# Kernel optimization log

Hardware: AMD Instinct MI355X
Metric: run time of the kernel (lower is better)

Reference implementation:

```python
import jax, jax.numpy as jnp
import numpy as np

N_NODES = 50000
N_EDGES = 800000
D_IN = 128
D_HID = 128
D_OUT = 64


def sage_conv(x, edge_index, W_l, b_l, W_r):
    # PyG SAGEConv (mean aggr): out = lin_l(mean_{j in N(i)} x_j) + lin_r(x_i)
    src, dst = edge_index[0], edge_index[1]
    msgs = x[src]  # [E, d] gather of source-node features
    summed = jax.ops.segment_sum(msgs, dst, num_segments=x.shape[0])
    deg = jax.ops.segment_sum(jnp.ones((edge_index.shape[1],), x.dtype), dst,
                              num_segments=x.shape[0])
    agg = summed / jnp.maximum(deg, 1.0)[:, None]  # nodes w/o in-edges -> 0
    return agg @ W_l + b_l + x @ W_r


def setup_inputs() -> dict:
    key = jax.random.key(0)
    ks = jax.random.split(key, 12)
    x = jax.random.normal(ks[0], (N_NODES, D_IN), dtype=jnp.float32)
    edge_index = jax.random.randint(ks[1], (2, N_EDGES), 0, N_NODES, dtype=jnp.int32)

    def glorot(k, shape):
        fan_in, fan_out = shape
        lim = (6.0 / (fan_in + fan_out)) ** 0.5
        return jax.random.uniform(k, shape, jnp.float32, -lim, lim)

    dims = [(D_IN, D_HID), (D_HID, D_HID), (D_HID, D_OUT)]
    params = {}
    for i, (din, dout) in enumerate(dims):
        params[f"Wl{i}"] = glorot(ks[2 + 3 * i], (din, dout))
        params[f"bl{i}"] = jnp.zeros((dout,), jnp.float32)
        params[f"Wr{i}"] = glorot(ks[3 + 3 * i], (din, dout))
    return {"x": x, "edge_index": edge_index, **params}


def reference(x, edge_index, Wl0, bl0, Wr0, Wl1, bl1, Wr1, Wl2, bl2, Wr2):
    # eval mode: dropout is identity
    h = jax.nn.relu(sage_conv(x, edge_index, Wl0, bl0, Wr0))
    h = jax.nn.relu(sage_conv(h, edge_index, Wl1, bl1, Wr1))
    out = sage_conv(h, edge_index, Wl2, bl2, Wr2)
    return out
```

## Files before the change

kernel.cpp:

```cpp
#include <hip/hip_runtime.h>

#define NN 50000
#define NE 800000
#define DK 128
#define NN_PAD 50048

#define SW 7
#define SUBCAP 20
#define CAP2 64

#define NPB 128
#define NBKT 391
#define BKTCAP 4096

#define AGG_BLOCKS 1568

typedef __attribute__((ext_vector_type(8))) short bf16x8;
typedef __attribute__((ext_vector_type(4))) float f32x4;
typedef __attribute__((ext_vector_type(2))) int   i32x2;
typedef __attribute__((ext_vector_type(4))) int   i32x4;
typedef __attribute__((ext_vector_type(4))) unsigned u32x4;
typedef __attribute__((ext_vector_type(8))) unsigned short u16x8;

__device__ inline unsigned short f2bf(float f) {
    unsigned u = __builtin_bit_cast(unsigned, f);
    u = (u + 0x7FFFu + ((u >> 16) & 1u)) >> 16;
    return (unsigned short)u;
}
__device__ inline float bfhi2f(unsigned u) {
    return __builtin_bit_cast(float, u & 0xFFFF0000u);
}
__device__ inline float bflo2f(unsigned u) {
    return __builtin_bit_cast(float, u << 16);
}
__device__ inline int clampn(int v) {
    return v >= NN ? NN - 1 : v;
}
__device__ inline void acc16(float* acc, u32x4 v) {
    acc[0] += bflo2f(v.x); acc[1] += bfhi2f(v.x);
    acc[2] += bflo2f(v.y); acc[3] += bfhi2f(v.y);
    acc[4] += bflo2f(v.z); acc[5] += bfhi2f(v.z);
    acc[6] += bflo2f(v.w); acc[7] += bfhi2f(v.w);
}


__global__ __launch_bounds__(256) void zero_int(int* __restrict__ p, int n) {
    int i = blockIdx.x * 256 + threadIdx.x;
    if (i < n) p[i] = 0;
}

__global__ __launch_bounds__(256) void partition_edges(const int* __restrict__ src,
                                                       const int* __restrict__ dst,
                                                       int* __restrict__ gcount,
                                                       unsigned* __restrict__ bucketbuf) {
    __shared__ int hist[NBKT];
    __shared__ int cur[NBKT];
    __shared__ int base[NBKT];
    int tid = threadIdx.x;
    for (int i = tid; i < NBKT; i += 256) { hist[i] = 0; cur[i] = 0; }
    __syncthreads();

    unsigned rec[8];
    int bkt[8];
    int e0 = (blockIdx.x * 256 + tid) * 8;
    bool valid = e0 < NE;
    if (valid) {
        i32x4 sa = __builtin_nontemporal_load((const i32x4*)(src + e0));
        i32x4 sb = __builtin_nontemporal_load((const i32x4*)(src + e0 + 4));
        i32x4 da = __builtin_nontemporal_load((const i32x4*)(dst + e0));
        i32x4 db = __builtin_nontemporal_load((const i32x4*)(dst + e0 + 4));
        int ss[8] = {sa.x, sa.y, sa.z, sa.w, sb.x, sb.y, sb.z, sb.w};
        int dd[8] = {da.x, da.y, da.z, da.w, db.x, db.y, db.z, db.w};
        #pragma unroll
        for (int k = 0; k < 8; ++k) {
            bkt[k] = dd[k] >> 7;
            rec[k] = (unsigned)ss[k] | ((unsigned)(dd[k] & 127) << 16);
            atomicAdd(&hist[bkt[k]], 1);
        }
    }
    __syncthreads();
    for (int i = tid; i < NBKT; i += 256)
        base[i] = atomicAdd(&gcount[i], hist[i]);
    __syncthreads();
    if (valid) {
        #pragma unroll
        for (int k = 0; k < 8; ++k) {
            int pos = base[bkt[k]] + atomicAdd(&cur[bkt[k]], 1);
            if (pos < BKTCAP)
                bucketbuf[(size_t)bkt[k] * BKTCAP + pos] = rec[k];
        }
    }
}

__global__ __launch_bounds__(256) void build_lists(const int* __restrict__ gcount,
                                                   const unsigned* __restrict__ bucketbuf,
                                                   unsigned short* __restrict__ eidx2,
                                                   int* __restrict__ deg) {
    __shared__ unsigned short list[NPB * CAP2];
    __shared__ int cnt[NPB * 8];
    __shared__ int cur[NPB * 8];
    __shared__ int off_[NPB * 8];
    int b = blockIdx.x, tid = threadIdx.x;
    int n0 = b << 7;
    int cntE = gcount[b];
    if (cntE > BKTCAP) cntE = BKTCAP;

    for (int i = tid; i < NPB * 8; i += 256) { cnt[i] = 0; cur[i] = 0; }
    u32x4* l4 = (u32x4*)list;
    for (int i = tid; i < NPB * CAP2 / 8; i += 256)
        l4[i] = (u32x4){0u, 0u, 0u, 0u};
    __syncthreads();

    const unsigned* bb = bucketbuf + (size_t)b * BKTCAP;
    for (int i = tid; i < cntE; i += 256) {
        unsigned r = bb[i];
        int nl = r >> 16;
        int w  = (r & 0xFFFFu) >> 13;
        atomicAdd(&cnt[nl * 8 + w], 1);
    }
    __syncthreads();

    if (tid < NPB) {
        int run = 0, dt = 0;
        #pragma unroll
        for (int w = 0; w < SW; ++w) {
            int c = cnt[tid * 8 + w];
            dt += c;
            off_[tid * 8 + w] = run;
            run += (c < SUBCAP) ? c : SUBCAP;
        }
        if (n0 + tid < NN) deg[n0 + tid] = dt;
    }
    __syncthreads();

    for (int i = tid; i < cntE; i += 256) {
        unsigned r = bb[i];
        int s  = (int)(r & 0xFFFFu);
        int nl = r >> 16;
        int w  = s >> 13;
        int slot = atomicAdd(&cur[nl * 8 + w], 1);
        int pos  = off_[nl * 8 + w] + slot;
        if (slot < SUBCAP && pos < CAP2)
            list[nl * CAP2 + pos] = (unsigned short)s;
    }
    __syncthreads();

    int nvalid = NN - n0;
    if (nvalid > NPB) nvalid = NPB;
    u32x4* out4 = (u32x4*)(eidx2 + (size_t)n0 * CAP2);
    for (int i = tid; i < nvalid * (CAP2 / 8); i += 256)
        __builtin_nontemporal_store(l4[i], out4 + i);
}


__global__ __launch_bounds__(256) void convert_bf16(const float* __restrict__ x,
                                                    unsigned short* __restrict__ xb) {
    long long i = (long long)(blockIdx.x * 256 + threadIdx.x) * 8;
    if (i >= (long long)NN * DK) return;
    f32x4 a = __builtin_nontemporal_load((const f32x4*)(x + i));
    f32x4 b = __builtin_nontemporal_load((const f32x4*)(x + i + 4));
    union { unsigned short us[8]; u32x4 u4; } o;
    o.us[0] = f2bf(a.x); o.us[1] = f2bf(a.y); o.us[2] = f2bf(a.z); o.us[3] = f2bf(a.w);
    o.us[4] = f2bf(b.x); o.us[5] = f2bf(b.y); o.us[6] = f2bf(b.z); o.us[7] = f2bf(b.w);
    *(u32x4*)(xb + i) = o.u4;
}


__global__ __launch_bounds__(256) void pack_w(const float* __restrict__ Wl,
                                              const float* __restrict__ Wr,
                                              unsigned short* __restrict__ Wpack,
                                              int N) {
    int tid = blockIdx.x * 256 + threadIdx.x;
    if (tid >= N * 32) return;
    int l  = tid & 63;
    int ks = (tid >> 6) & 7;
    int nt = tid >> 9;
    int n  = nt * 16 + (l & 15);
    int kb = ks * 32 + (l >> 4) * 8;
    union { unsigned short us[8]; u32x4 u4; } o;
    #pragma unroll
    for (int j = 0; j < 8; ++j) {
        int k = kb + j;
        float w = (k < 128) ? Wl[k * N + n] : Wr[(k - 128) * N + n];
        o.us[j] = f2bf(w);
    }
    *(u32x4*)(Wpack + (size_t)tid * 8) = o.u4;
}

__global__ __launch_bounds__(256) void pack_w1(const float* __restrict__ W,
                                               unsigned short* __restrict__ Wpack) {
    int tid = blockIdx.x * 256 + threadIdx.x;
    if (tid >= 1024) return;
    int l  = tid & 63;
    int ks = (tid >> 6) & 3;
    int nt = tid >> 8;
    int n  = nt * 16 + (l & 15);
    int kb = ks * 32 + (l >> 4) * 8;
    union { unsigned short us[8]; u32x4 u4; } o;
    #pragma unroll
    for (int j = 0; j < 8; ++j) o.us[j] = f2bf(W[(kb + j) * 64 + n]);
    *(u32x4*)(Wpack + (size_t)tid * 8) = o.u4;
}

template <int S>
__global__ __launch_bounds__(256) void aggregate(const unsigned short* __restrict__ h,
                                                 const unsigned short* __restrict__ eidx2,
                                                 const int* __restrict__ deg,
                                                 unsigned short* __restrict__ agg) {
    constexpr int NPB_ = 256 / S;
    int g    = threadIdx.x / S;
    int lane = threadIdx.x % S;
    const u32x4* h4 = (const u32x4*)h;
    for (int base = 0; base < NN; base += AGG_BLOCKS * NPB_) {
        int node = base + blockIdx.x * NPB_ + g;
        if (node >= NN) continue;
        int d   = deg[node];
        int cap = (d < CAP2) ? d : CAP2;
        const unsigned short* el = eidx2 + (size_t)node * CAP2;
        float acc[8] = {0.f, 0.f, 0.f, 0.f, 0.f, 0.f, 0.f, 0.f};
        int j = 0;
        for (; j + 7 < cap; j += 8) {
            u16x8 i8 = *(const u16x8*)(el + j);
            u32x4 v[8];
            #pragma unroll
            for (int q = 0; q < 8; ++q)
                v[q] = h4[(size_t)clampn((int)i8[q]) * S + lane];
            #pragma unroll
            for (int q = 0; q < 8; ++q) acc16(acc, v[q]);
        }
        for (; j + 3 < cap; j += 4) {
            u32x4 v[4];
            #pragma unroll
            for (int q = 0; q < 4; ++q)
                v[q] = h4[(size_t)clampn((int)el[j + q]) * S + lane];
            #pragma unroll
            for (int q = 0; q < 4; ++q) acc16(acc, v[q]);
        }
        for (; j < cap; ++j)
            acc16(acc, h4[(size_t)clampn((int)el[j]) * S + lane]);
        float r = 1.0f / (float)(d > 0 ? d : 1);
        union { unsigned short us[8]; u32x4 u4; } o;
        #pragma unroll
        for (int k = 0; k < 8; ++k) o.us[k] = f2bf(acc[k] * r);
        __builtin_nontemporal_store(o.u4, (u32x4*)agg + (size_t)node * S + lane);
    }
}


template <int N, bool RELU, bool OUT_BF16>
__global__ __launch_bounds__(256) void gemm_mfma(const unsigned short* __restrict__ agg,
                                                 const unsigned short* __restrict__ h,
                                                 const unsigned short* __restrict__ Wpack,
                                                 const float* __restrict__ bias,
                                                 void* __restrict__ outp) {
    __shared__ unsigned short Wlds[N * 256];
    int tid = threadIdx.x;
    {
        const u32x4* wg = (const u32x4*)Wpack;
        u32x4* wl = (u32x4*)Wlds;
        #pragma unroll
        for (int i = tid; i < N * 32; i += 256) wl[i] = wg[i];
    }
    __syncthreads();

    int wave = tid >> 6, lane = tid & 63;
    int m = lane & 15, quad = lane >> 4;
    int row0 = blockIdx.x * 128 + wave * 16;

    const unsigned short* arow = agg + (size_t)(row0 + m) * 128 + quad * 8;
    const unsigned short* hrow = h   + (size_t)(row0 + m) * 128 + quad * 8;

    f32x4 acc0[N / 16] = {};
    f32x4 acc1[N / 16] = {};
    #pragma unroll
    for (int ks = 0; ks < 8; ++ks) {
        const unsigned short* s = (ks < 4) ? (arow + ks * 32) : (hrow + (ks - 4) * 32);
        bf16x8 a0 = *(const bf16x8*)s;
        bf16x8 a1 = *(const bf16x8*)(s + 64 * 128);
        #pragma unroll
        for (int nt = 0; nt < N / 16; ++nt) {
            bf16x8 b = *(const bf16x8*)&Wlds[((nt * 8 + ks) * 64 + lane) * 8];
            acc0[nt] = __builtin_amdgcn_mfma_f32_16x16x32_bf16(a0, b, acc0[nt], 0, 0, 0);
            acc1[nt] = __builtin_amdgcn_mfma_f32_16x16x32_bf16(a1, b, acc1[nt], 0, 0, 0);
        }
    }

    #pragma unroll
    for (int t = 0; t < 2; ++t) {
        #pragma unroll
        for (int nt = 0; nt < N / 16; ++nt) {
            int n = nt * 16 + m;
            float bv = bias[n];
            #pragma unroll
            for (int r = 0; r < 4; ++r) {
                int row = row0 + t * 64 + quad * 4 + r;
                if (row < NN) {
                    float v = (t == 0 ? acc0[nt][r] : acc1[nt][r]) + bv;
                    if (RELU) v = fmaxf(v, 0.f);
                    if (OUT_BF16)
                        ((unsigned short*)outp)[(size_t)row * N + n] = f2bf(v);
                    else
                        ((float*)outp)[(size_t)row * N + n] = v;
                }
            }
        }
    }
}

__global__ __launch_bounds__(256) void gemm_single(const unsigned short* __restrict__ h,
                                                   const unsigned short* __restrict__ Wpack,
                                                   unsigned short* __restrict__ P) {
    __shared__ unsigned short Wlds[64 * 128];
    int tid = threadIdx.x;
    {
        const u32x4* wg = (const u32x4*)Wpack;
        u32x4* wl = (u32x4*)Wlds;
        #pragma unroll
        for (int i = tid; i < 1024; i += 256) wl[i] = wg[i];
    }
    __syncthreads();

    int wave = tid >> 6, lane = tid & 63;
    int m = lane & 15, quad = lane >> 4;
    int row0 = blockIdx.x * 128 + wave * 16;

    const unsigned short* hrow = h + (size_t)(row0 + m) * 128 + quad * 8;

    f32x4 acc0[4] = {};
    f32x4 acc1[4] = {};
    #pragma unroll
    for (int ks = 0; ks < 4; ++ks) {
        bf16x8 a0 = *(const bf16x8*)(hrow + ks * 32);
        bf16x8 a1 = *(const bf16x8*)(hrow + ks * 32 + 64 * 128);
        #pragma unroll
        for (int nt = 0; nt < 4; ++nt) {
            bf16x8 b = *(const bf16x8*)&Wlds[((nt * 4 + ks) * 64 + lane) * 8];
            acc0[nt] = __builtin_amdgcn_mfma_f32_16x16x32_bf16(a0, b, acc0[nt], 0, 0, 0);
            acc1[nt] = __builtin_amdgcn_mfma_f32_16x16x32_bf16(a1, b, acc1[nt], 0, 0, 0);
        }
    }

    #pragma unroll
    for (int t = 0; t < 2; ++t) {
        #pragma unroll
        for (int nt = 0; nt < 4; ++nt) {
            int n = nt * 16 + m;
            #pragma unroll
            for (int r = 0; r < 4; ++r) {
                int row = row0 + t * 64 + quad * 4 + r;
                if (row < NN)
                    P[(size_t)row * 64 + n] = f2bf(t == 0 ? acc0[nt][r] : acc1[nt][r]);
            }
        }
    }
}

__global__ __launch_bounds__(256) void gemm_final(const unsigned short* __restrict__ h,
                                                  const unsigned short* __restrict__ Wpack,
                                                  const float* __restrict__ bias,
                                                  const unsigned short* __restrict__ aggP,
                                                  float* __restrict__ outp) {
    __shared__ unsigned short Wlds[64 * 128];
    int tid = threadIdx.x;
    {
        const u32x4* wg = (const u32x4*)Wpack;
        u32x4* wl = (u32x4*)Wlds;
        #pragma unroll
        for (int i = tid; i < 1024; i += 256) wl[i] = wg[i];
    }
    __syncthreads();

    int wave = tid >> 6, lane = tid & 63;
    int m = lane & 15, quad = lane >> 4;
    int row0 = blockIdx.x * 128 + wave * 16;

    const unsigned short* hrow = h + (size_t)(row0 + m) * 128 + quad * 8;

    f32x4 acc0[4] = {};
    f32x4 acc1[4] = {};
    #pragma unroll
    for (int ks = 0; ks < 4; ++ks) {
        bf16x8 a0 = *(const bf16x8*)(hrow + ks * 32);
        bf16x8 a1 = *(const bf16x8*)(hrow + ks * 32 + 64 * 128);
        #pragma unroll
        for (int nt = 0; nt < 4; ++nt) {
            bf16x8 b = *(const bf16x8*)&Wlds[((nt * 4 + ks) * 64 + lane) * 8];
            acc0[nt] = __builtin_amdgcn_mfma_f32_16x16x32_bf16(a0, b, acc0[nt], 0, 0, 0);
            acc1[nt] = __builtin_amdgcn_mfma_f32_16x16x32_bf16(a1, b, acc1[nt], 0, 0, 0);
        }
    }

    #pragma unroll
    for (int t = 0; t < 2; ++t) {
        #pragma unroll
        for (int nt = 0; nt < 4; ++nt) {
            int n = nt * 16 + m;
            float bv = bias[n];
            #pragma unroll
            for (int r = 0; r < 4; ++r) {
                int row = row0 + t * 64 + quad * 4 + r;
                if (row < NN) {
                    float av = bflo2f((unsigned)aggP[(size_t)row * 64 + n]);
                    outp[(size_t)row * 64 + n] =
                        (t == 0 ? acc0[nt][r] : acc1[nt][r]) + bv + av;
                }
            }
        }
    }
}


static inline size_t align256(size_t x) { return (x + 255) & ~(size_t)255; }

extern "C" void kernel_launch(void* const* d_in, const int* in_sizes, int n_in,
                              void* d_out, int out_size, void* d_ws, size_t ws_size,
                              hipStream_t stream) {
    const float* x    = (const float*)d_in[0];
    const int*   ei   = (const int*)d_in[1];
    const int*   esrc = ei;
    const int*   edst = ei + NE;
    const float* Wl0 = (const float*)d_in[2];
    const float* bl0 = (const float*)d_in[3];
    const float* Wr0 = (const float*)d_in[4];
    const float* Wl1 = (const float*)d_in[5];
    const float* bl1 = (const float*)d_in[6];
    const float* Wr1 = (const float*)d_in[7];
    const float* Wl2 = (const float*)d_in[8];
    const float* bl2 = (const float*)d_in[9];
    const float* Wr2 = (const float*)d_in[10];

    char* ws = (char*)d_ws;
    size_t off = 0;
    int* gcount = (int*)(ws + off);             off = align256(off + (size_t)NBKT * 4);
    unsigned* bucketbuf = (unsigned*)(ws + off);
    off = align256(off + (size_t)NBKT * BKTCAP * 4);
    unsigned short* eidx2 = (unsigned short*)(ws + off);
    off = align256(off + (size_t)NN * CAP2 * 2);
    int* deg = (int*)(ws + off);                off = align256(off + (size_t)NN * 4);
    unsigned short* xb   = (unsigned short*)(ws + off); off = align256(off + (size_t)NN_PAD * DK * 2);
    unsigned short* bAgg = (unsigned short*)(ws + off); off = align256(off + (size_t)NN_PAD * DK * 2);
    unsigned short* bH   = (unsigned short*)(ws + off); off = align256(off + (size_t)NN_PAD * DK * 2);
    unsigned short* P2   = (unsigned short*)(ws + off); off = align256(off + (size_t)NN_PAD * 64 * 2);
    unsigned short* aggP = (unsigned short*)(ws + off); off = align256(off + (size_t)NN_PAD * 64 * 2);
    unsigned short* Wp0  = (unsigned short*)(ws + off); off = align256(off + (size_t)256 * 128 * 2);
    unsigned short* Wp1  = (unsigned short*)(ws + off); off = align256(off + (size_t)256 * 128 * 2);
    unsigned short* Wp2l = (unsigned short*)(ws + off); off = align256(off + (size_t)128 * 64 * 2);
    unsigned short* Wp2r = (unsigned short*)(ws + off); off = align256(off + (size_t)128 * 64 * 2);

    zero_int<<<(NBKT + 255) / 256, 256, 0, stream>>>(gcount, NBKT);
    partition_edges<<<(NE / 8 + 255) / 256, 256, 0, stream>>>(esrc, edst, gcount, bucketbuf);
    build_lists<<<NBKT, 256, 0, stream>>>(gcount, bucketbuf, eidx2, deg);

    convert_bf16<<<(NN * DK / 8 + 255) / 256, 256, 0, stream>>>(x, xb);
    pack_w<<<(128 * 32 + 255) / 256, 256, 0, stream>>>(Wl0, Wr0, Wp0, 128);
    pack_w<<<(128 * 32 + 255) / 256, 256, 0, stream>>>(Wl1, Wr1, Wp1, 128);
    pack_w1<<<4, 256, 0, stream>>>(Wl2, Wp2l);
    pack_w1<<<4, 256, 0, stream>>>(Wr2, Wp2r);

    const int GEMM_GRID = NN_PAD / 128;

    aggregate<16><<<AGG_BLOCKS, 256, 0, stream>>>(xb, eidx2, deg, bAgg);
    gemm_mfma<128, true, true><<<GEMM_GRID, 256, 0, stream>>>(bAgg, xb, Wp0, bl0, bH);

    aggregate<16><<<AGG_BLOCKS, 256, 0, stream>>>(bH, eidx2, deg, bAgg);
    gemm_mfma<128, true, true><<<GEMM_GRID, 256, 0, stream>>>(bAgg, bH, Wp1, bl1, xb);

    gemm_single<<<GEMM_GRID, 256, 0, stream>>>(xb, Wp2l, P2);
    aggregate<8><<<AGG_BLOCKS, 256, 0, stream>>>(P2, eidx2, deg, aggP);
    gemm_final<<<GEMM_GRID, 256, 0, stream>>>(xb, Wp2r, bl2, aggP, (float*)d_out);
}
```

Baseline: 250.4 us.

## Fuse neighbor aggregation into GEMM kernels and merge prep launches

Each SAGE layer's mean aggregation now runs inside the GEMM kernel, writing aggregated rows into LDS instead of a global buffer, and layer 2's projection by Wl2 is fused into the layer-1 epilogue. The final layer aggregates the projected P2 in LDS and adds it directly. The weight packing, bf16 conversion and counter zeroing are merged into one prep launch, and an XCD-aware block swizzle is added. This removes intermediate global round trips and several launches. In exchange, aggregation parallelism drops to 391 blocks with serial passes, weights are read from global memory instead of LDS, and the larger LDS footprint may lower occupancy.

```diff
diff --git a/kernel.cpp b/kernel.cpp
--- a/kernel.cpp
+++ b/kernel.cpp
@@ -13,7 +13,7 @@
 #define NBKT 391
 #define BKTCAP 4096
 
-#define AGG_BLOCKS 1568
+#define GEMM_GRID 391
 
 typedef __attribute__((ext_vector_type(8))) short bf16x8;
 typedef __attribute__((ext_vector_type(4))) float f32x4;
@@ -42,12 +42,12 @@
     acc[4] += bflo2f(v.z); acc[5] += bfhi2f(v.z);
     acc[6] += bflo2f(v.w); acc[7] += bfhi2f(v.w);
 }
-
-
-__global__ __launch_bounds__(256) void zero_int(int* __restrict__ p, int n) {
-    int i = blockIdx.x * 256 + threadIdx.x;
-    if (i < n) p[i] = 0;
-}
+__device__ inline int xcd_swz(int b, int nwg) {
+    int q = nwg >> 3, r = nwg & 7;
+    int xc = b & 7, y = b >> 3;
+    return (xc < r ? xc * (q + 1) : r * (q + 1) + (xc - r) * q) + y;
+}
+
 
 __global__ __launch_bounds__(256) void partition_edges(const int* __restrict__ src,
                                                        const int* __restrict__ dst,
@@ -152,179 +152,257 @@
         __builtin_nontemporal_store(l4[i], out4 + i);
 }
 
-
-__global__ __launch_bounds__(256) void convert_bf16(const float* __restrict__ x,
-                                                    unsigned short* __restrict__ xb) {
-    long long i = (long long)(blockIdx.x * 256 + threadIdx.x) * 8;
-    if (i >= (long long)NN * DK) return;
-    f32x4 a = __builtin_nontemporal_load((const f32x4*)(x + i));
-    f32x4 b = __builtin_nontemporal_load((const f32x4*)(x + i + 4));
-    union { unsigned short us[8]; u32x4 u4; } o;
-    o.us[0] = f2bf(a.x); o.us[1] = f2bf(a.y); o.us[2] = f2bf(a.z); o.us[3] = f2bf(a.w);
-    o.us[4] = f2bf(b.x); o.us[5] = f2bf(b.y); o.us[6] = f2bf(b.z); o.us[7] = f2bf(b.w);
-    *(u32x4*)(xb + i) = o.u4;
-}
-
-
-__global__ __launch_bounds__(256) void pack_w(const float* __restrict__ Wl,
-                                              const float* __restrict__ Wr,
-                                              unsigned short* __restrict__ Wpack,
-                                              int N) {
-    int tid = blockIdx.x * 256 + threadIdx.x;
-    if (tid >= N * 32) return;
-    int l  = tid & 63;
-    int ks = (tid >> 6) & 7;
-    int nt = tid >> 9;
-    int n  = nt * 16 + (l & 15);
-    int kb = ks * 32 + (l >> 4) * 8;
-    union { unsigned short us[8]; u32x4 u4; } o;
-    #pragma unroll
-    for (int j = 0; j < 8; ++j) {
-        int k = kb + j;
-        float w = (k < 128) ? Wl[k * N + n] : Wr[(k - 128) * N + n];
-        o.us[j] = f2bf(w);
-    }
-    *(u32x4*)(Wpack + (size_t)tid * 8) = o.u4;
-}
-
-__global__ __launch_bounds__(256) void pack_w1(const float* __restrict__ W,
-                                               unsigned short* __restrict__ Wpack) {
-    int tid = blockIdx.x * 256 + threadIdx.x;
-    if (tid >= 1024) return;
-    int l  = tid & 63;
-    int ks = (tid >> 6) & 3;
-    int nt = tid >> 8;
-    int n  = nt * 16 + (l & 15);
-    int kb = ks * 32 + (l >> 4) * 8;
-    union { unsigned short us[8]; u32x4 u4; } o;
-    #pragma unroll
-    for (int j = 0; j < 8; ++j) o.us[j] = f2bf(W[(kb + j) * 64 + n]);
-    *(u32x4*)(Wpack + (size_t)tid * 8) = o.u4;
-}
-
-template <int S>
-__global__ __launch_bounds__(256) void aggregate(const unsigned short* __restrict__ h,
-                                                 const unsigned short* __restrict__ eidx2,
-                                                 const int* __restrict__ deg,
-                                                 unsigned short* __restrict__ agg) {
-    constexpr int NPB_ = 256 / S;
-    int g    = threadIdx.x / S;
-    int lane = threadIdx.x % S;
-    const u32x4* h4 = (const u32x4*)h;
-    for (int base = 0; base < NN; base += AGG_BLOCKS * NPB_) {
-        int node = base + blockIdx.x * NPB_ + g;
-        if (node >= NN) continue;
-        int d   = deg[node];
-        int cap = (d < CAP2) ? d : CAP2;
-        const unsigned short* el = eidx2 + (size_t)node * CAP2;
-        float acc[8] = {0.f, 0.f, 0.f, 0.f, 0.f, 0.f, 0.f, 0.f};
-        int j = 0;
-        for (; j + 7 < cap; j += 8) {
-            u16x8 i8 = *(const u16x8*)(el + j);
-            u32x4 v[8];
-            #pragma unroll
-            for (int q = 0; q < 8; ++q)
-                v[q] = h4[(size_t)clampn((int)i8[q]) * S + lane];
-            #pragma unroll
-            for (int q = 0; q < 8; ++q) acc16(acc, v[q]);
-        }
-        for (; j + 3 < cap; j += 4) {
-            u32x4 v[4];
-            #pragma unroll
-            for (int q = 0; q < 4; ++q)
-                v[q] = h4[(size_t)clampn((int)el[j + q]) * S + lane];
-            #pragma unroll
-            for (int q = 0; q < 4; ++q) acc16(acc, v[q]);
-        }
-        for (; j < cap; ++j)
-            acc16(acc, h4[(size_t)clampn((int)el[j]) * S + lane]);
-        float r = 1.0f / (float)(d > 0 ? d : 1);
+__global__ __launch_bounds__(256) void prep(const float* __restrict__ x,
+                                            unsigned short* __restrict__ xb,
+                                            const float* __restrict__ Wl0,
+                                            const float* __restrict__ Wr0,
+                                            unsigned short* __restrict__ Wp0,
+                                            const float* __restrict__ Wl1,
+                                            const float* __restrict__ Wr1,
+                                            unsigned short* __restrict__ Wp1,
+                                            const float* __restrict__ Wl2,
+                                            unsigned short* __restrict__ Wp2l,
+                                            const float* __restrict__ Wr2,
+                                            unsigned short* __restrict__ Wp2r,
+                                            int* __restrict__ gcount) {
+    int b = blockIdx.x;
+    if (b < NN_PAD * DK / 8 / 256) {
+        long long i = ((long long)b * 256 + threadIdx.x) * 8;
+        if (i < (long long)NN * DK) {
+            f32x4 a = __builtin_nontemporal_load((const f32x4*)(x + i));
+            f32x4 c = __builtin_nontemporal_load((const f32x4*)(x + i + 4));
+            union { unsigned short us[8]; u32x4 u4; } o;
+            o.us[0] = f2bf(a.x); o.us[1] = f2bf(a.y); o.us[2] = f2bf(a.z); o.us[3] = f2bf(a.w);
+            o.us[4] = f2bf(c.x); o.us[5] = f2bf(c.y); o.us[6] = f2bf(c.z); o.us[7] = f2bf(c.w);
+            *(u32x4*)(xb + i) = o.u4;
+        } else {
+            *(u32x4*)(xb + i) = (u32x4){0u, 0u, 0u, 0u};
+        }
+        return;
+    }
+    b -= NN_PAD * DK / 8 / 256;
+    if (b < 32) {
+        const float* Wl = (b < 16) ? Wl0 : Wl1;
+        const float* Wr = (b < 16) ? Wr0 : Wr1;
+        unsigned short* Wp = (b < 16) ? Wp0 : Wp1;
+        int tid = (b & 15) * 256 + threadIdx.x;
+        int l  = tid & 63;
+        int ks = (tid >> 6) & 7;
+        int nt = tid >> 9;
+        int n  = nt * 16 + (l & 15);
+        int kb = ks * 32 + (l >> 4) * 8;
         union { unsigned short us[8]; u32x4 u4; } o;
         #pragma unroll
-        for (int k = 0; k < 8; ++k) o.us[k] = f2bf(acc[k] * r);
-        __builtin_nontemporal_store(o.u4, (u32x4*)agg + (size_t)node * S + lane);
-    }
-}
-
-
-template <int N, bool RELU, bool OUT_BF16>
-__global__ __launch_bounds__(256) void gemm_mfma(const unsigned short* __restrict__ agg,
-                                                 const unsigned short* __restrict__ h,
-                                                 const unsigned short* __restrict__ Wpack,
-                                                 const float* __restrict__ bias,
-                                                 void* __restrict__ outp) {
-    __shared__ unsigned short Wlds[N * 256];
+        for (int j = 0; j < 8; ++j) {
+            int k = kb + j;
+            float w = (k < 128) ? Wl[k * 128 + n] : Wr[(k - 128) * 128 + n];
+            o.us[j] = f2bf(w);
+        }
+        *(u32x4*)(Wp + (size_t)tid * 8) = o.u4;
+        return;
+    }
+    b -= 32;
+    if (b < 8) {
+        const float* W = (b < 4) ? Wl2 : Wr2;
+        unsigned short* Wp = (b < 4) ? Wp2l : Wp2r;
+        int tid = (b & 3) * 256 + threadIdx.x;
+        int l  = tid & 63;
+        int ks = (tid >> 6) & 3;
+        int nt = tid >> 8;
+        int n  = nt * 16 + (l & 15);
+        int kb = ks * 32 + (l >> 4) * 8;
+        union { unsigned short us[8]; u32x4 u4; } o;
+        #pragma unroll
+        for (int j = 0; j < 8; ++j) o.us[j] = f2bf(W[(kb + j) * 64 + n]);
+        *(u32x4*)(Wp + (size_t)tid * 8) = o.u4;
+        return;
+    }
+    for (int i = threadIdx.x; i < NBKT; i += 256) gcount[i] = 0;
+}
+
+template <bool P2OUT>
+__global__ __launch_bounds__(256) void fused_layer(const unsigned short* __restrict__ h,
+                                                   const unsigned short* __restrict__ eidx2,
+                                                   const int* __restrict__ deg,
+                                                   const unsigned short* __restrict__ Wpack,
+                                                   const float* __restrict__ bias,
+                                                   unsigned short* __restrict__ out,
+                                                   const unsigned short* __restrict__ Wp2,
+                                                   unsigned short* __restrict__ P2) {
+    constexpr int RS = 136;
+    __shared__ unsigned short Alds[128 * RS];
     int tid = threadIdx.x;
+    int bid = xcd_swz(blockIdx.x, GEMM_GRID);
+    int node0 = bid * 128;
+
     {
-        const u32x4* wg = (const u32x4*)Wpack;
-        u32x4* wl = (u32x4*)Wlds;
-        #pragma unroll
-        for (int i = tid; i < N * 32; i += 256) wl[i] = wg[i];
+        int g = tid >> 4, lane = tid & 15;
+        const u32x4* h4 = (const u32x4*)h;
+        for (int pass = 0; pass < 8; ++pass) {
+            int nl = pass * 16 + g;
+            int node = node0 + nl;
+            int d = (node < NN) ? deg[node] : 0;
+            int cap = (d < CAP2) ? d : CAP2;
+            const unsigned short* el = eidx2 + (size_t)node * CAP2;
+            float acc[8] = {0.f, 0.f, 0.f, 0.f, 0.f, 0.f, 0.f, 0.f};
+            int j = 0;
+            for (; j + 7 < cap; j += 8) {
+                u16x8 i8 = *(const u16x8*)(el + j);
+                u32x4 v[8];
+                #pragma unroll
+                for (int q = 0; q < 8; ++q)
+                    v[q] = h4[(size_t)clampn((int)i8[q]) * 16 + lane];
+                #pragma unroll
+                for (int q = 0; q < 8; ++q) acc16(acc, v[q]);
+            }
+            for (; j + 3 < cap; j += 4) {
+                u32x4 v[4];
+                #pragma unroll
+                for (int q = 0; q < 4; ++q)
+                    v[q] = h4[(size_t)clampn((int)el[j + q]) * 16 + lane];
+                #pragma unroll
+                for (int q = 0; q < 4; ++q) acc16(acc, v[q]);
+            }
+            for (; j < cap; ++j)
+                acc16(acc, h4[(size_t)clampn((int)el[j]) * 16 + lane]);
+            float rd = 1.0f / (float)(d > 0 ? d : 1);
+            union { unsigned short us[8]; u32x4 u4; } o;
+            #pragma unroll
+            for (int k = 0; k < 8; ++k) o.us[k] = f2bf(acc[k] * rd);
+            *(u32x4*)&Alds[nl * RS + lane * 8] = o.u4;
+        }
     }
     __syncthreads();
 
     int wave = tid >> 6, lane = tid & 63;
     int m = lane & 15, quad = lane >> 4;
-    int row0 = blockIdx.x * 128 + wave * 16;
-
-    const unsigned short* arow = agg + (size_t)(row0 + m) * 128 + quad * 8;
-    const unsigned short* hrow = h   + (size_t)(row0 + m) * 128 + quad * 8;
-
-    f32x4 acc0[N / 16] = {};
-    f32x4 acc1[N / 16] = {};
+    int r0 = wave * 16;
+    const unsigned short* a0p  = &Alds[(r0 + m) * RS + quad * 8];
+    const unsigned short* hrow = h + (size_t)(node0 + r0 + m) * 128 + quad * 8;
+
+    f32x4 acc0[8] = {};
+    f32x4 acc1[8] = {};
     #pragma unroll
     for (int ks = 0; ks < 8; ++ks) {
-        const unsigned short* s = (ks < 4) ? (arow + ks * 32) : (hrow + (ks - 4) * 32);
-        bf16x8 a0 = *(const bf16x8*)s;
-        bf16x8 a1 = *(const bf16x8*)(s + 64 * 128);
-        #pragma unroll
-        for (int nt = 0; nt < N / 16; ++nt) {
-            bf16x8 b = *(const bf16x8*)&Wlds[((nt * 8 + ks) * 64 + lane) * 8];
-            acc0[nt] = __builtin_amdgcn_mfma_f32_16x16x32_bf16(a0, b, acc0[nt], 0, 0, 0);
-            acc1[nt] = __builtin_amdgcn_mfma_f32_16x16x32_bf16(a1, b, acc1[nt], 0, 0, 0);
+        bf16x8 a0, a1;
+        if (ks < 4) {
+            a0 = *(const bf16x8*)(a0p + ks * 32);
+            a1 = *(const bf16x8*)(a0p + 64 * RS + ks * 32);
+        } else {
+            a0 = *(const bf16x8*)(hrow + (ks - 4) * 32);
+            a1 = *(const bf16x8*)(hrow + 64 * 128 + (ks - 4) * 32);
+        }
+        #pragma unroll
+        for (int nt = 0; nt < 8; ++nt) {
+            bf16x8 bfr = *(const bf16x8*)&Wpack[((size_t)(nt * 8 + ks) * 64 + lane) * 8];
+            acc0[nt] = __builtin_amdgcn_mfma_f32_16x16x32_bf16(a0, bfr, acc0[nt], 0, 0, 0);
+            acc1[nt] = __builtin_amdgcn_mfma_f32_16x16x32_bf16(a1, bfr, acc1[nt], 0, 0, 0);
         }
     }
 
     #pragma unroll
     for (int t = 0; t < 2; ++t) {
         #pragma unroll
-        for (int nt = 0; nt < N / 16; ++nt) {
+        for (int nt = 0; nt < 8; ++nt) {
             int n = nt * 16 + m;
             float bv = bias[n];
             #pragma unroll
             for (int r = 0; r < 4; ++r) {
-                int row = row0 + t * 64 + quad * 4 + r;
-                if (row < NN) {
-                    float v = (t == 0 ? acc0[nt][r] : acc1[nt][r]) + bv;
-                    if (RELU) v = fmaxf(v, 0.f);
-                    if (OUT_BF16)
-                        ((unsigned short*)outp)[(size_t)row * N + n] = f2bf(v);
-                    else
-                        ((float*)outp)[(size_t)row * N + n] = v;
+                int rl = t * 64 + r0 + quad * 4 + r;
+                float v = fmaxf((t == 0 ? acc0[nt][r] : acc1[nt][r]) + bv, 0.f);
+                unsigned short us = f2bf(v);
+                out[(size_t)(node0 + rl) * 128 + n] = us;
+                if constexpr (P2OUT) Alds[rl * RS + n] = us;
+            }
+        }
+    }
+
+    if constexpr (P2OUT) {
+        f32x4 p0[4] = {};
+        f32x4 p1[4] = {};
+        #pragma unroll
+        for (int ks = 0; ks < 4; ++ks) {
+            bf16x8 a0 = *(const bf16x8*)&Alds[(r0 + m) * RS + ks * 32 + quad * 8];
+            bf16x8 a1 = *(const bf16x8*)&Alds[(64 + r0 + m) * RS + ks * 32 + quad * 8];
+            #pragma unroll
+            for (int nt = 0; nt < 4; ++nt) {
+                bf16x8 bfr = *(const bf16x8*)&Wp2[((size_t)(nt * 4 + ks) * 64 + lane) * 8];
+                p0[nt] = __builtin_amdgcn_mfma_f32_16x16x32_bf16(a0, bfr, p0[nt], 0, 0, 0);
+                p1[nt] = __builtin_amdgcn_mfma_f32_16x16x32_bf16(a1, bfr, p1[nt], 0, 0, 0);
+            }
+        }
+        #pragma unroll
+        for (int t = 0; t < 2; ++t) {
+            #pragma unroll
+            for (int nt = 0; nt < 4; ++nt) {
+                int n = nt * 16 + m;
+                #pragma unroll
+                for (int r = 0; r < 4; ++r) {
+                    int rl = t * 64 + r0 + quad * 4 + r;
+                    P2[(size_t)(node0 + rl) * 64 + n] =
+                        f2bf(t == 0 ? p0[nt][r] : p1[nt][r]);
                 }
             }
         }
     }
 }
 
-__global__ __launch_bounds__(256) void gemm_single(const unsigned short* __restrict__ h,
-                                                   const unsigned short* __restrict__ Wpack,
-                                                   unsigned short* __restrict__ P) {
-    __shared__ unsigned short Wlds[64 * 128];
+__global__ __launch_bounds__(256) void fused_final(const unsigned short* __restrict__ h,
+                                                   const unsigned short* __restrict__ P2,
+                                                   const unsigned short* __restrict__ eidx2,
+                                                   const int* __restrict__ deg,
+                                                   const unsigned short* __restrict__ Wp2r,
+                                                   const float* __restrict__ bias,
+                                                   float* __restrict__ outp) {
+    constexpr int RS2 = 72;
+    __shared__ unsigned short Plds[128 * RS2];
     int tid = threadIdx.x;
+    int bid = xcd_swz(blockIdx.x, GEMM_GRID);
+    int node0 = bid * 128;
+
     {
-        const u32x4* wg = (const u32x4*)Wpack;
-        u32x4* wl = (u32x4*)Wlds;
-        #pragma unroll
-        for (int i = tid; i < 1024; i += 256) wl[i] = wg[i];
+        int g = tid >> 3, lane = tid & 7;
+        const u32x4* p4 = (const u32x4*)P2;
+        for (int pass = 0; pass < 4; ++pass) {
+            int nl = pass * 32 + g;
+            int node = node0 + nl;
+            int d = (node < NN) ? deg[node] : 0;
+            int cap = (d < CAP2) ? d : CAP2;
+            const unsigned short* el = eidx2 + (size_t)node * CAP2;
+            float acc[8] = {0.f, 0.f, 0.f, 0.f, 0.f, 0.f, 0.f, 0.f};
+            int j = 0;
+            for (; j + 7 < cap; j += 8) {
+                u16x8 i8 = *(const u16x8*)(el + j);
+                u32x4 v[8];
+                #pragma unroll
+                for (int q = 0; q < 8; ++q)
+                    v[q] = p4[(size_t)clampn((int)i8[q]) * 8 + lane];
+                #pragma unroll
+                for (int q = 0; q < 8; ++q) acc16(acc, v[q]);
+            }
+            for (; j + 3 < cap; j += 4) {
+                u32x4 v[4];
+                #pragma unroll
+                for (int q = 0; q < 4; ++q)
+                    v[q] = p4[(size_t)clampn((int)el[j + q]) * 8 + lane];
+                #pragma unroll
+                for (int q = 0; q < 4; ++q) acc16(acc, v[q]);
+            }
+            for (; j < cap; ++j)
+                acc16(acc, p4[(size_t)clampn((int)el[j]) * 8 + lane]);
+            float rd = 1.0f / (float)(d > 0 ? d : 1);
+            union { unsigned short us[8]; u32x4 u4; } o;
+            #pragma unroll
+            for (int k = 0; k < 8; ++k) o.us[k] = f2bf(acc[k] * rd);
+            *(u32x4*)&Plds[nl * RS2 + lane * 8] = o.u4;
+        }
     }
     __syncthreads();
 
     int wave = tid >> 6, lane = tid & 63;
     int m = lane & 15, quad = lane >> 4;
-    int row0 = blockIdx.x * 128 + wave * 16;
-
-    const unsigned short* hrow = h + (size_t)(row0 + m) * 128 + quad * 8;
+    int r0 = wave * 16;
+    const unsigned short* hrow = h + (size_t)(node0 + r0 + m) * 128 + quad * 8;
 
     f32x4 acc0[4] = {};
     f32x4 acc1[4] = {};
@@ -334,59 +412,9 @@
         bf16x8 a1 = *(const bf16x8*)(hrow + ks * 32 + 64 * 128);
         #pragma unroll
         for (int nt = 0; nt < 4; ++nt) {
-            bf16x8 b = *(const bf16x8*)&Wlds[((nt * 4 + ks) * 64 + lane) * 8];
-            acc0[nt] = __builtin_amdgcn_mfma_f32_16x16x32_bf16(a0, b, acc0[nt], 0, 0, 0);
-            acc1[nt] = __builtin_amdgcn_mfma_f32_16x16x32_bf16(a1, b, acc1[nt], 0, 0, 0);
-        }
-    }
-
-    #pragma unroll
-    for (int t = 0; t < 2; ++t) {
-        #pragma unroll
-        for (int nt = 0; nt < 4; ++nt) {
-            int n = nt * 16 + m;
-            #pragma unroll
-            for (int r = 0; r < 4; ++r) {
-                int row = row0 + t * 64 + quad * 4 + r;
-                if (row < NN)
-                    P[(size_t)row * 64 + n] = f2bf(t == 0 ? acc0[nt][r] : acc1[nt][r]);
-            }
-        }
-    }
-}
-
-__global__ __launch_bounds__(256) void gemm_final(const unsigned short* __restrict__ h,
-                                                  const unsigned short* __restrict__ Wpack,
-                                                  const float* __restrict__ bias,
-                                                  const unsigned short* __restrict__ aggP,
-                                                  float* __restrict__ outp) {
-    __shared__ unsigned short Wlds[64 * 128];
-    int tid = threadIdx.x;
-    {
-        const u32x4* wg = (const u32x4*)Wpack;
-        u32x4* wl = (u32x4*)Wlds;
-        #pragma unroll
-        for (int i = tid; i < 1024; i += 256) wl[i] = wg[i];
-    }
-    __syncthreads();
-
-    int wave = tid >> 6, lane = tid & 63;
-    int m = lane & 15, quad = lane >> 4;
-    int row0 = blockIdx.x * 128 + wave * 16;
-
-    const unsigned short* hrow = h + (size_t)(row0 + m) * 128 + quad * 8;
-
-    f32x4 acc0[4] = {};
-    f32x4 acc1[4] = {};
-    #pragma unroll
-    for (int ks = 0; ks < 4; ++ks) {
-        bf16x8 a0 = *(const bf16x8*)(hrow + ks * 32);
-        bf16x8 a1 = *(const bf16x8*)(hrow + ks * 32 + 64 * 128);
-        #pragma unroll
-        for (int nt = 0; nt < 4; ++nt) {
-            bf16x8 b = *(const bf16x8*)&Wlds[((nt * 4 + ks) * 64 + lane) * 8];
-            acc0[nt] = __builtin_amdgcn_mfma_f32_16x16x32_bf16(a0, b, acc0[nt], 0, 0, 0);
-            acc1[nt] = __builtin_amdgcn_mfma_f32_16x16x32_bf16(a1, b, acc1[nt], 0, 0, 0);
+            bf16x8 bfr = *(const bf16x8*)&Wp2r[((size_t)(nt * 4 + ks) * 64 + lane) * 8];
+            acc0[nt] = __builtin_amdgcn_mfma_f32_16x16x32_bf16(a0, bfr, acc0[nt], 0, 0, 0);
+            acc1[nt] = __builtin_amdgcn_mfma_f32_16x16x32_bf16(a1, bfr, acc1[nt], 0, 0, 0);
         }
     }
 
@@ -398,9 +426,10 @@
             float bv = bias[n];
             #pragma unroll
             for (int r = 0; r < 4; ++r) {
-                int row = row0 + t * 64 + quad * 4 + r;
+                int rl = t * 64 + r0 + quad * 4 + r;
+                int row = node0 + rl;
                 if (row < NN) {
-                    float av = bflo2f((unsigned)aggP[(size_t)row * 64 + n]);
+                    float av = bflo2f((unsigned)Plds[rl * RS2 + n]);
                     outp[(size_t)row * 64 + n] =
                         (t == 0 ? acc0[nt][r] : acc1[nt][r]) + bv + av;
                 }
@@ -438,34 +467,22 @@
     off = align256(off + (size_t)NN * CAP2 * 2);
     int* deg = (int*)(ws + off);                off = align256(off + (size_t)NN * 4);
     unsigned short* xb   = (unsigned short*)(ws + off); off = align256(off + (size_t)NN_PAD * DK * 2);
-    unsigned short* bAgg = (unsigned short*)(ws + off); off = align256(off + (size_t)NN_PAD * DK * 2);
     unsigned short* bH   = (unsigned short*)(ws + off); off = align256(off + (size_t)NN_PAD * DK * 2);
     unsigned short* P2   = (unsigned short*)(ws + off); off = align256(off + (size_t)NN_PAD * 64 * 2);
-    unsigned short* aggP = (unsigned short*)(ws + off); off = align256(off + (size_t)NN_PAD * 64 * 2);
     unsigned short* Wp0  = (unsigned short*)(ws + off); off = align256(off + (size_t)256 * 128 * 2);
     unsigned short* Wp1  = (unsigned short*)(ws + off); off = align256(off + (size_t)256 * 128 * 2);
     unsigned short* Wp2l = (unsigned short*)(ws + off); off = align256(off + (size_t)128 * 64 * 2);
     unsigned short* Wp2r = (unsigned short*)(ws + off); off = align256(off + (size_t)128 * 64 * 2);
 
-    zero_int<<<(NBKT + 255) / 256, 256, 0, stream>>>(gcount, NBKT);
+    prep<<<NN_PAD * DK / 8 / 256 + 32 + 8 + 1, 256, 0, stream>>>(
+        x, xb, Wl0, Wr0, Wp0, Wl1, Wr1, Wp1, Wl2, Wp2l, Wr2, Wp2r, gcount);
     partition_edges<<<(NE / 8 + 255) / 256, 256, 0, stream>>>(esrc, edst, gcount, bucketbuf);
     build_lists<<<NBKT, 256, 0, stream>>>(gcount, bucketbuf, eidx2, deg);
 
-    convert_bf16<<<(NN * DK / 8 + 255) / 256, 256, 0, stream>>>(x, xb);
-    pack_w<<<(128 * 32 + 255) / 256, 256, 0, stream>>>(Wl0, Wr0, Wp0, 128);
-    pack_w<<<(128 * 32 + 255) / 256, 256, 0, stream>>>(Wl1, Wr1, Wp1, 128);
-    pack_w1<<<4, 256, 0, stream>>>(Wl2, Wp2l);
-    pack_w1<<<4, 256, 0, stream>>>(Wr2, Wp2r);
-
-    const int GEMM_GRID = NN_PAD / 128;
-
-    aggregate<16><<<AGG_BLOCKS, 256, 0, stream>>>(xb, eidx2, deg, bAgg);
-    gemm_mfma<128, true, true><<<GEMM_GRID, 256, 0, stream>>>(bAgg, xb, Wp0, bl0, bH);
-
-    aggregate<16><<<AGG_BLOCKS, 256, 0, stream>>>(bH, eidx2, deg, bAgg);
-    gemm_mfma<128, true, true><<<GEMM_GRID, 256, 0, stream>>>(bAgg, bH, Wp1, bl1, xb);
-
-    gemm_single<<<GEMM_GRID, 256, 0, stream>>>(xb, Wp2l, P2);
-    aggregate<8><<<AGG_BLOCKS, 256, 0, stream>>>(P2, eidx2, deg, aggP);
-    gemm_final<<<GEMM_GRID, 256, 0, stream>>>(xb, Wp2r, bl2, aggP, (float*)d_out);
-}
+    fused_layer<false><<<GEMM_GRID, 256, 0, stream>>>(xb, eidx2, deg, Wp0, bl0, bH,
+                                                      nullptr, nullptr);
+    fused_layer<true><<<GEMM_GRID, 256, 0, stream>>>(bH, eidx2, deg, Wp1, bl1, xb,
+                                                     Wp2l, P2);
+    fused_final<<<GEMM_GRID, 256, 0, stream>>>(xb, P2, eidx2, deg, Wp2r, bl2,
+                                               (float*)d_out);
+}
```

Measured after the change: 272.1 us. +8.7%, slower.
